# Performance work log

Hardware: AMD Instinct MI355X
Metric: run time of the kernel (lower is better)

Reference implementation:

```python
import jax, jax.numpy as jnp
import numpy as np

NIN, DIM, NHEAD = 512, 64, 8
B, N = 2, 2048

def setup_inputs() -> dict:
    key = jax.random.key(0)
    ks = jax.random.split(key, 7)
    s = 1.0 / np.sqrt(NIN)  # torch Linear default init range
    out_f = DIM * NHEAD
    return {
        "x": jax.random.normal(ks[0], (B, N, NIN), dtype=jnp.float32),
        "Wq": jax.random.uniform(ks[1], (out_f, NIN), jnp.float32, -s, s),
        "bq": jax.random.uniform(ks[2], (out_f,), jnp.float32, -s, s),
        "Wk": jax.random.uniform(ks[3], (out_f, NIN), jnp.float32, -s, s),
        "bk": jax.random.uniform(ks[4], (out_f,), jnp.float32, -s, s),
        "Wv": jax.random.uniform(ks[5], (out_f, NIN), jnp.float32, -s, s),
        "bv": jax.random.uniform(ks[6], (out_f,), jnp.float32, -s, s),
    }

def reference(x, Wq, bq, Wk, bk, Wv, bv):
    b, n, nin = x.shape
    scale = DIM ** (-0.5)
    # torch: self.qs(x).view(nhead, B, N, dim) -- a FLAT reshape, not a transpose
    q = (x @ Wq.T + bq).reshape(NHEAD, b, n, DIM)
    k = (x @ Wk.T + bk).reshape(NHEAD, b, n, DIM)
    v = (x @ Wv.T + bv).reshape(NHEAD, b, n, DIM)
    # no softmax in the original module; mask path is a no-op (masked_fill not in-place)
    att = jnp.einsum('hbid,hbjd->hbij', q, k) * scale  # [h,b,n,n]
    out = jnp.einsum('hbij,hbjd->hbid', att, v)        # [h,b,n,d]
    out = jnp.transpose(out, (1, 2, 3, 0))             # [b,n,d,h]
    return out.reshape(b, n, -1)
```

## Files before the change

kernel.cpp:

```cpp
#include <hip/hip_runtime.h>
#include <stdint.h>

#define CHELEM 131072

typedef __attribute__((ext_vector_type(4))) float   f32x4;
typedef __attribute__((ext_vector_type(8))) short   bh8;
typedef __attribute__((ext_vector_type(4))) unsigned short u16x4;
typedef __attribute__((ext_vector_type(8))) unsigned short u16x8;
typedef unsigned short u16;

__device__ inline u16 f2bf(float f) {
    union { float f; uint32_t u; } v; v.f = f;
    uint32_t u = v.u;
    u += 0x7FFF + ((u >> 16) & 1);
    return (u16)(u >> 16);
}

__global__ __launch_bounds__(256) void k1_qkv(
        const float* __restrict__ x,
        const float* __restrict__ Wq, const float* __restrict__ Wk,
        const float* __restrict__ Wv,
        const float* __restrict__ bq, const float* __restrict__ bk,
        const float* __restrict__ bv,
        u16* __restrict__ Qb, u16* __restrict__ Kb, u16* __restrict__ Vb) {
    __shared__ u16 smem[12288];
    u16* lA = smem;
    u16* lB = smem + 4096;
    const int tid  = threadIdx.x;
    const int lane = tid & 63, wid = tid >> 6;
    const int wr = wid >> 1, wc = wid & 1;
    const int swz  = (blockIdx.x & 7) * 96 + (blockIdx.x >> 3);
    const int mb = swz / 12, nb = swz % 12;
    const int w    = nb >> 2;
    const int nloc = (nb & 3) * 128;
    const float4* x4 = (const float4*)x;
    const float4* W4 = (const float4*)((w == 0) ? Wq : ((w == 1) ? Wk : Wv));
    const float*  bias = (w == 0) ? bq : ((w == 1) ? bk : bv);
    u16*          out  = (w == 0) ? Qb : ((w == 1) ? Kb : Vb);
    const int m0 = mb * 64;

    f32x4 acc[2][4] = {};

    for (int kb = 0; kb < 8; ++kb) {
        __syncthreads();
        const int k4 = kb * 16;
        float4 ra[4], rb[8];
#pragma unroll
        for (int v = 0; v < 4; ++v) {
            const int idx = v * 256 + tid;
            ra[v] = x4[(size_t)(m0 + (idx >> 4)) * 128 + k4 + (idx & 15)];
        }
#pragma unroll
        for (int v = 0; v < 8; ++v) {
            const int idx = v * 256 + tid;
            rb[v] = W4[(size_t)(nloc + (idx >> 4)) * 128 + k4 + (idx & 15)];
        }
#pragma unroll
        for (int v = 0; v < 4; ++v) {
            const int idx = v * 256 + tid;
            u16x4 o;
            o[0] = f2bf(ra[v].x); o[1] = f2bf(ra[v].y);
            o[2] = f2bf(ra[v].z); o[3] = f2bf(ra[v].w);
            *(u16x4*)&lA[(idx >> 4) * 64 + (idx & 15) * 4] = o;
        }
#pragma unroll
        for (int v = 0; v < 8; ++v) {
            const int idx = v * 256 + tid;
            u16x4 o;
            o[0] = f2bf(rb[v].x); o[1] = f2bf(rb[v].y);
            o[2] = f2bf(rb[v].z); o[3] = f2bf(rb[v].w);
            *(u16x4*)&lB[(idx >> 4) * 64 + (idx & 15) * 4] = o;
        }
        __syncthreads();
#pragma unroll
        for (int ks = 0; ks < 2; ++ks) {
            const int kk = ks * 32 + (lane >> 4) * 8;
            bh8 a[2], b[4];
#pragma unroll
            for (int i = 0; i < 2; ++i)
                a[i] = *(const bh8*)&lA[(wr * 32 + i * 16 + (lane & 15)) * 64 + kk];
#pragma unroll
            for (int j = 0; j < 4; ++j)
                b[j] = *(const bh8*)&lB[(wc * 64 + j * 16 + (lane & 15)) * 64 + kk];
#pragma unroll
            for (int i = 0; i < 2; ++i)
#pragma unroll
                for (int j = 0; j < 4; ++j)
                    acc[i][j] = __builtin_amdgcn_mfma_f32_16x16x32_bf16(a[i], b[j], acc[i][j], 0, 0, 0);
        }
    }

    if (w == 0) {
#pragma unroll
        for (int i = 0; i < 2; ++i) {
            const int row_base = m0 + wr * 32 + i * 16 + ((lane >> 4) * 4);
#pragma unroll
            for (int j = 0; j < 4; ++j) {
                const int col = nloc + wc * 64 + j * 16 + (lane & 15);
                const float bv_ = bias[col];
#pragma unroll
                for (int r = 0; r < 4; ++r)
                    out[(size_t)(row_base + r) * 512 + col] = f2bf(acc[i][j][r] + bv_);
            }
        }
    } else {
        __syncthreads();
        u16 (*tile)[130] = (u16(*)[130])smem;
#pragma unroll
        for (int i = 0; i < 2; ++i) {
            const int ml = wr * 32 + i * 16 + ((lane >> 4) * 4);
#pragma unroll
            for (int j = 0; j < 4; ++j) {
                const int nl = wc * 64 + j * 16 + (lane & 15);
                const float bv_ = bias[nloc + nl];
#pragma unroll
                for (int r = 0; r < 4; ++r)
                    tile[ml + r][nl] = f2bf(acc[i][j][r] + bv_);
            }
        }
        __syncthreads();
        const int ncol  = tid & 127;
        const int mhalf = tid >> 7;
        const int g = (nb & 3) * 2 + (ncol >> 6);
        const int d = ncol & 63;
        const int c = mb >> 2;
        const int qbase = (mb & 3) * 64 + mhalf * 32;
        u16* dst = out + (size_t)c * CHELEM + d * 2048 + g * 256 + qbase;
#pragma unroll
        for (int v = 0; v < 4; ++v) {
            u16x8 t;
#pragma unroll
            for (int j = 0; j < 8; ++j)
                t[j] = tile[mhalf * 32 + v * 8 + j][ncol];
            *(u16x8*)(dst + v * 8) = t;
        }
    }
}

__global__ __launch_bounds__(256) void k2_pmat(
        const u16* __restrict__ Kt2, const u16* __restrict__ Vt2,
        u16* __restrict__ Pb) {
    __shared__ float red[4][16][16];
    const int tid = threadIdx.x;
    const int lane = tid & 63, w = tid >> 6;
    const int c   = blockIdx.x & 15;
    const int sub = blockIdx.x >> 4;
    const int dq = sub >> 2, eq = sub & 3;
    const u16* Vc = Vt2 + (size_t)c * CHELEM;
    const u16* Kc = Kt2 + (size_t)c * CHELEM;
    const int krow = lane & 15;
    const int arow = (dq * 16 + krow) * 2048;
    const int brow = (eq * 16 + krow) * 2048;
    const int kb = w * 512 + (lane >> 4) * 8;

    f32x4 acc = {};
#pragma unroll
    for (int kt = 0; kt < 16; ++kt) {
        const int k0 = kb + kt * 32;
        bh8 a = *(const bh8*)&Vc[arow + k0];
        bh8 b = *(const bh8*)&Kc[brow + k0];
        acc = __builtin_amdgcn_mfma_f32_16x16x32_bf16(a, b, acc, 0, 0, 0);
    }
#pragma unroll
    for (int r = 0; r < 4; ++r)
        red[w][(lane >> 4) * 4 + r][lane & 15] = acc[r];
    __syncthreads();
    const int row = tid >> 4, col = tid & 15;
    float s = red[0][row][col] + red[1][row][col] + red[2][row][col] + red[3][row][col];
    Pb[c * 4096 + (dq * 16 + row) * 64 + eq * 16 + col] = f2bf(s * 0.125f);
}

__global__ __launch_bounds__(256) void k3_out(
        const u16* __restrict__ Qb, const u16* __restrict__ Pb,
        float* __restrict__ outp) {
    const int tid = threadIdx.x;
    const int lane = tid & 63, w = tid >> 6;
    const int bb = blockIdx.x >> 6;
    const int ib = blockIdx.x & 63;
    const int i0 = ib * 32 + (w >> 1) * 16;
    const int dbase = (w & 1) * 32;
    const int krow = lane & 15;
    const int koff = (lane >> 4) * 8;

    f32x4 acc[8][2] = {};
#pragma unroll
    for (int h = 0; h < 8; ++h) {
        const int c = h * 2 + bb;
        const u16* Qc = Qb + (size_t)c * CHELEM;
        const u16* Pc = Pb + c * 4096;
#pragma unroll
        for (int ks = 0; ks < 2; ++ks) {
            bh8 a = *(const bh8*)&Qc[(i0 + krow) * 64 + ks * 32 + koff];
#pragma unroll
            for (int nf = 0; nf < 2; ++nf) {
                bh8 b = *(const bh8*)&Pc[(dbase + nf * 16 + krow) * 64 + ks * 32 + koff];
                acc[h][nf] = __builtin_amdgcn_mfma_f32_16x16x32_bf16(a, b, acc[h][nf], 0, 0, 0);
            }
        }
    }
    const int orow_base = bb * 2048 + ib * 32 + (w >> 1) * 16 + (lane >> 4) * 4;
#pragma unroll
    for (int nf = 0; nf < 2; ++nf) {
        const int d = dbase + nf * 16 + (lane & 15);
#pragma unroll
        for (int r = 0; r < 4; ++r) {
            f32x4 lo = {acc[0][nf][r], acc[1][nf][r], acc[2][nf][r], acc[3][nf][r]};
            f32x4 hi = {acc[4][nf][r], acc[5][nf][r], acc[6][nf][r], acc[7][nf][r]};
            float* dst = outp + (size_t)(orow_base + r) * 512 + d * 8;
            *(f32x4*)dst = lo;
            *(f32x4*)(dst + 4) = hi;
        }
    }
}

extern "C" void kernel_launch(void* const* d_in, const int* in_sizes, int n_in,
                              void* d_out, int out_size, void* d_ws, size_t ws_size,
                              hipStream_t stream) {
    const float* x  = (const float*)d_in[0];
    const float* Wq = (const float*)d_in[1];
    const float* bq = (const float*)d_in[2];
    const float* Wk = (const float*)d_in[3];
    const float* bk = (const float*)d_in[4];
    const float* Wv = (const float*)d_in[5];
    const float* bv = (const float*)d_in[6];
    float* outp = (float*)d_out;

    u16* Qb = (u16*)d_ws;
    u16* Kb = Qb + 2097152;
    u16* Vb = Kb + 2097152;
    u16* Pb = Vb + 2097152;

    k1_qkv<<<768, 256, 0, stream>>>(x, Wq, Wk, Wv, bq, bk, bv, Qb, Kb, Vb);
    k2_pmat<<<256, 256, 0, stream>>>(Kb, Vb, Pb);
    k3_out<<<128, 256, 0, stream>>>(Qb, Pb, outp);
}
```

Before: 43.14 us.

## Double-buffer QKV projection LDS, use packed bf16 convert, split output kernel finer

The QKV projection kernel now double-buffers its LDS tiles. It issues global loads for the next K-slice before computing on the current one, which removes one barrier per iteration and hides load latency. The float-to-bf16 conversion switches from software rounding to the hardware v_cvt_pk_bf16_f32 instruction, and launch bounds ask for 3 blocks per CU. The output kernel gives each block a 16-row strip with one d-fragment per wave, doubling the grid to 256 blocks for better CU coverage. The cost is twice the LDS per block in k1 and less Q reuse per block in k3.

```diff
diff --git a/kernel.cpp b/kernel.cpp
--- a/kernel.cpp
+++ b/kernel.cpp
@@ -16,16 +16,20 @@
     return (u16)(u >> 16);
 }
 
-__global__ __launch_bounds__(256) void k1_qkv(
+__device__ inline uint32_t cvt2(float lo, float hi) {
+    uint32_t r;
+    asm("v_cvt_pk_bf16_f32 %0, %1, %2" : "=v"(r) : "v"(lo), "v"(hi));
+    return r;
+}
+
+__global__ __launch_bounds__(256, 3) void k1_qkv(
         const float* __restrict__ x,
         const float* __restrict__ Wq, const float* __restrict__ Wk,
         const float* __restrict__ Wv,
         const float* __restrict__ bq, const float* __restrict__ bk,
         const float* __restrict__ bv,
         u16* __restrict__ Qb, u16* __restrict__ Kb, u16* __restrict__ Vb) {
-    __shared__ u16 smem[12288];
-    u16* lA = smem;
-    u16* lB = smem + 4096;
+    __shared__ u16 smem[2][12288];
     const int tid  = threadIdx.x;
     const int lane = tid & 63, wid = tid >> 6;
     const int wr = wid >> 1, wc = wid & 1;
@@ -40,11 +44,10 @@
     const int m0 = mb * 64;
 
     f32x4 acc[2][4] = {};
-
-    for (int kb = 0; kb < 8; ++kb) {
-        __syncthreads();
+    float4 ra[4], rb[8];
+
+    auto issue = [&](int kb) {
         const int k4 = kb * 16;
-        float4 ra[4], rb[8];
 #pragma unroll
         for (int v = 0; v < 4; ++v) {
             const int idx = v * 256 + tid;
@@ -55,39 +58,56 @@
             const int idx = v * 256 + tid;
             rb[v] = W4[(size_t)(nloc + (idx >> 4)) * 128 + k4 + (idx & 15)];
         }
+    };
+    auto cvt_write = [&](int b) {
+        u16* bA = smem[b];
+        u16* bB = smem[b] + 4096;
 #pragma unroll
         for (int v = 0; v < 4; ++v) {
             const int idx = v * 256 + tid;
-            u16x4 o;
-            o[0] = f2bf(ra[v].x); o[1] = f2bf(ra[v].y);
-            o[2] = f2bf(ra[v].z); o[3] = f2bf(ra[v].w);
-            *(u16x4*)&lA[(idx >> 4) * 64 + (idx & 15) * 4] = o;
+            uint32_t p0 = cvt2(ra[v].x, ra[v].y);
+            uint32_t p1 = cvt2(ra[v].z, ra[v].w);
+            uint2 pk; pk.x = p0; pk.y = p1;
+            *(uint2*)&bA[(idx >> 4) * 64 + (idx & 15) * 4] = pk;
         }
 #pragma unroll
         for (int v = 0; v < 8; ++v) {
             const int idx = v * 256 + tid;
-            u16x4 o;
-            o[0] = f2bf(rb[v].x); o[1] = f2bf(rb[v].y);
-            o[2] = f2bf(rb[v].z); o[3] = f2bf(rb[v].w);
-            *(u16x4*)&lB[(idx >> 4) * 64 + (idx & 15) * 4] = o;
-        }
-        __syncthreads();
+            uint32_t p0 = cvt2(rb[v].x, rb[v].y);
+            uint32_t p1 = cvt2(rb[v].z, rb[v].w);
+            uint2 pk; pk.x = p0; pk.y = p1;
+            *(uint2*)&bB[(idx >> 4) * 64 + (idx & 15) * 4] = pk;
+        }
+    };
+    auto compute = [&](int b) {
+        const u16* bA = smem[b];
+        const u16* bB = smem[b] + 4096;
 #pragma unroll
         for (int ks = 0; ks < 2; ++ks) {
             const int kk = ks * 32 + (lane >> 4) * 8;
-            bh8 a[2], b[4];
+            bh8 a[2], bfr[4];
 #pragma unroll
             for (int i = 0; i < 2; ++i)
-                a[i] = *(const bh8*)&lA[(wr * 32 + i * 16 + (lane & 15)) * 64 + kk];
+                a[i] = *(const bh8*)&bA[(wr * 32 + i * 16 + (lane & 15)) * 64 + kk];
 #pragma unroll
             for (int j = 0; j < 4; ++j)
-                b[j] = *(const bh8*)&lB[(wc * 64 + j * 16 + (lane & 15)) * 64 + kk];
+                bfr[j] = *(const bh8*)&bB[(wc * 64 + j * 16 + (lane & 15)) * 64 + kk];
 #pragma unroll
             for (int i = 0; i < 2; ++i)
 #pragma unroll
                 for (int j = 0; j < 4; ++j)
-                    acc[i][j] = __builtin_amdgcn_mfma_f32_16x16x32_bf16(a[i], b[j], acc[i][j], 0, 0, 0);
-        }
+                    acc[i][j] = __builtin_amdgcn_mfma_f32_16x16x32_bf16(a[i], bfr[j], acc[i][j], 0, 0, 0);
+        }
+    };
+
+    issue(0);
+    cvt_write(0);
+    __syncthreads();
+    for (int kb = 0; kb < 8; ++kb) {
+        if (kb < 7) issue(kb + 1);
+        compute(kb & 1);
+        if (kb < 7) cvt_write((kb + 1) & 1);
+        __syncthreads();
     }
 
     if (w == 0) {
@@ -104,7 +124,6 @@
             }
         }
     } else {
-        __syncthreads();
         u16 (*tile)[130] = (u16(*)[130])smem;
 #pragma unroll
         for (int i = 0; i < 2; ++i) {
@@ -175,14 +194,15 @@
         float* __restrict__ outp) {
     const int tid = threadIdx.x;
     const int lane = tid & 63, w = tid >> 6;
-    const int bb = blockIdx.x >> 6;
-    const int ib = blockIdx.x & 63;
-    const int i0 = ib * 32 + (w >> 1) * 16;
-    const int dbase = (w & 1) * 32;
+    const int bid = blockIdx.x;
+    const int bb = bid >> 7;
+    const int ib = bid & 127;
+    const int i0 = ib * 16;
+    const int dbase = w * 16;
     const int krow = lane & 15;
     const int koff = (lane >> 4) * 8;
 
-    f32x4 acc[8][2] = {};
+    f32x4 acc[8] = {};
 #pragma unroll
     for (int h = 0; h < 8; ++h) {
         const int c = h * 2 + bb;
@@ -191,25 +211,19 @@
 #pragma unroll
         for (int ks = 0; ks < 2; ++ks) {
             bh8 a = *(const bh8*)&Qc[(i0 + krow) * 64 + ks * 32 + koff];
-#pragma unroll
-            for (int nf = 0; nf < 2; ++nf) {
-                bh8 b = *(const bh8*)&Pc[(dbase + nf * 16 + krow) * 64 + ks * 32 + koff];
-                acc[h][nf] = __builtin_amdgcn_mfma_f32_16x16x32_bf16(a, b, acc[h][nf], 0, 0, 0);
-            }
-        }
-    }
-    const int orow_base = bb * 2048 + ib * 32 + (w >> 1) * 16 + (lane >> 4) * 4;
-#pragma unroll
-    for (int nf = 0; nf < 2; ++nf) {
-        const int d = dbase + nf * 16 + (lane & 15);
-#pragma unroll
-        for (int r = 0; r < 4; ++r) {
-            f32x4 lo = {acc[0][nf][r], acc[1][nf][r], acc[2][nf][r], acc[3][nf][r]};
-            f32x4 hi = {acc[4][nf][r], acc[5][nf][r], acc[6][nf][r], acc[7][nf][r]};
-            float* dst = outp + (size_t)(orow_base + r) * 512 + d * 8;
-            *(f32x4*)dst = lo;
-            *(f32x4*)(dst + 4) = hi;
-        }
+            bh8 b = *(const bh8*)&Pc[(dbase + krow) * 64 + ks * 32 + koff];
+            acc[h] = __builtin_amdgcn_mfma_f32_16x16x32_bf16(a, b, acc[h], 0, 0, 0);
+        }
+    }
+    const int orow_base = bb * 2048 + i0 + (lane >> 4) * 4;
+    const int d = dbase + (lane & 15);
+#pragma unroll
+    for (int r = 0; r < 4; ++r) {
+        f32x4 lo = {acc[0][r], acc[1][r], acc[2][r], acc[3][r]};
+        f32x4 hi = {acc[4][r], acc[5][r], acc[6][r], acc[7][r]};
+        float* dst = outp + (size_t)(orow_base + r) * 512 + d * 8;
+        *(f32x4*)dst = lo;
+        *(f32x4*)(dst + 4) = hi;
     }
 }
 
@@ -232,5 +246,5 @@
 
     k1_qkv<<<768, 256, 0, stream>>>(x, Wq, Wk, Wv, bq, bk, bv, Qb, Kb, Vb);
     k2_pmat<<<256, 256, 0, stream>>>(Kb, Vb, Pb);
-    k3_out<<<128, 256, 0, stream>>>(Qb, Pb, outp);
-}
+    k3_out<<<256, 256, 0, stream>>>(Qb, Pb, outp);
+}
```

After: 37.80 us. 12.4% less time.
